# Kernel tuning notes

Measured on AMD Instinct MI355X. Metric: run time of the kernel, lower is better.

The kernel has to match this reference:

```python
import jax, jax.numpy as jnp
import numpy as np

B, T, V, E, H = 256, 512, 50000, 300, 128
NORM_GAIN = 0.8     # norm_gain fed at train time
FORGET_BIAS = 1.0
EPS = 1e-12         # tf.contrib.layers.layer_norm default epsilon


def setup_inputs() -> dict:
    key = jax.random.key(0)
    k1, k2, k3 = jax.random.split(key, 3)
    x = jax.random.randint(k1, (B, T), 0, V, dtype=jnp.int32)
    embed = jax.random.normal(k2, (V, E), dtype=jnp.float32)  # tf.random_normal stddev=1
    W = jax.random.normal(k3, (E + H, 4 * H), dtype=jnp.float32) / np.float32(np.sqrt(E + H))
    gains = jnp.full((5, H), NORM_GAIN, dtype=jnp.float32)   # i, j, f, o, cell-transform
    shifts = jnp.zeros((5, H), dtype=jnp.float32)
    return {"x": x, "embed": embed, "W": W, "gains": gains, "shifts": shifts}


def _ln(v, g, b):
    # layer norm over feature axis with learned gain/shift
    m = jnp.mean(v, axis=-1, keepdims=True)
    var = jnp.mean(jnp.square(v - m), axis=-1, keepdims=True)
    return (v - m) * jax.lax.rsqrt(var + EPS) * g + b


def reference(x, embed, W, gains, shifts):
    # embedding: einsum('abc,cd->abd', one_hot(x), embed) == embed[x]
    xe = jnp.take(embed, x, axis=0)            # [B, T, E]
    xe = jnp.transpose(xe, (1, 0, 2))          # [T, B, E] for scan
    c0 = jnp.zeros((x.shape[0], H), jnp.float32)
    h0 = c0

    def step(carry, x_t):
        c, h = carry
        z = jnp.concatenate([x_t, h], axis=-1) @ W      # [B, 4H], no bias
        i, j, f, o = jnp.split(z, 4, axis=-1)
        i = _ln(i, gains[0], shifts[0])
        j = _ln(j, gains[1], shifts[1])
        f = _ln(f, gains[2], shifts[2])
        o = _ln(o, gains[3], shifts[3])
        g = jax.nn.relu(j)                              # activation=tf.nn.relu
        new_c = c * jax.nn.sigmoid(f + FORGET_BIAS) + jax.nn.sigmoid(i) * g
        new_h = jax.nn.relu(_ln(new_c, gains[4], shifts[4])) * jax.nn.sigmoid(o)
        return (new_c, new_h), new_h

    _, ys = jax.lax.scan(step, (c0, h0), xe)            # ys: [T, B, H]
    return jnp.transpose(ys, (1, 0, 2))                 # [B, T, H]
```

## Files before the change

### kernel.cpp

```cpp
#include <hip/hip_runtime.h>
#include <math.h>

#define Bb   256
#define Tt   512
#define Vv   50000
#define Ee   300
#define Hh   128
#define G4   512
#define EPS  1e-12f
#define FBIAS 1.0f

typedef _Float16 half8 __attribute__((ext_vector_type(8)));
typedef float    f32x4 __attribute__((ext_vector_type(4)));

template <int CTRL>
__device__ inline float dpp_mov(float v) {
    return __int_as_float(
        __builtin_amdgcn_update_dpp(0, __float_as_int(v), CTRL, 0xF, 0xF, true));
}
__device__ inline float red16(float v) {
    v += dpp_mov<0xB1>(v);
    v += dpp_mov<0x4E>(v);
    v += dpp_mov<0x141>(v);
    v += dpp_mov<0x140>(v);
    return v;
}
__device__ inline float red64b(float v) {
    v = red16(v);
    v += dpp_mov<0x142>(v);
    v += dpp_mov<0x143>(v);
    return __int_as_float(__builtin_amdgcn_readlane(__float_as_int(v), 63));
}

__device__ inline void lds_barrier() {
    __builtin_amdgcn_sched_barrier(0);
    asm volatile("s_waitcnt lgkmcnt(0)" ::: "memory");
    __builtin_amdgcn_sched_barrier(0);
    __builtin_amdgcn_s_barrier();
    __builtin_amdgcn_sched_barrier(0);
}

__device__ inline float sigm(float v) {
    return __fdividef(1.0f, 1.0f + __expf(-v));
}

#define PROJ_TILES ((Vv + 31) / 32)

__global__ __launch_bounds__(512, 2) void embed_proj_mfma(
    const float* __restrict__ embed,
    const float* __restrict__ W,
    _Float16* __restrict__ P)
{
    __shared__ __align__(16) _Float16 A[32 * 320];

    const int tid  = threadIdx.x;
    const int wv   = tid >> 6;
    const int lane = tid & 63;
    const int p16  = lane & 15;
    const int gq   = lane >> 4;

    half8 bf[4][10];
    #pragma unroll
    for (int tt = 0; tt < 4; ++tt) {
        #pragma unroll
        for (int ks = 0; ks < 10; ++ks) {
            half8 h;
            #pragma unroll
            for (int j = 0; j < 8; ++j) {
                int k = ks * 32 + gq * 8 + j;
                h[j] = (k < Ee)
                     ? (_Float16)W[(size_t)k * G4 + wv * 64 + tt * 16 + p16]
                     : (_Float16)0.f;
            }
            bf[tt][ks] = h;
        }
    }

    char* const Ab = (char*)A;
    for (int i = tid; i < 32 * 10; i += 512) {
        int row = i / 10, m = i - row * 10;
        *(uint*)(Ab + ((row * 640 + 600 + m * 4) ^ ((row & 7) << 4))) = 0u;
    }
    __syncthreads();

    for (int mtile = blockIdx.x; mtile < PROJ_TILES; mtile += gridDim.x) {
        const int r0 = mtile * 32;

        for (int i = tid; i < 32 * 75; i += 512) {
            int row = i / 75, k4 = i - row * 75;
            int grow = r0 + row;
            float4 v = (grow < Vv) ? *(const float4*)&embed[(size_t)grow * Ee + k4 * 4]
                                   : (float4){0.f, 0.f, 0.f, 0.f};
            union { _Float16 h[4]; uint2 u; } pk;
            pk.h[0] = (_Float16)v.x; pk.h[1] = (_Float16)v.y;
            pk.h[2] = (_Float16)v.z; pk.h[3] = (_Float16)v.w;
            *(uint2*)(Ab + ((row * 640 + k4 * 8) ^ ((row & 7) << 4))) = pk.u;
        }
        __syncthreads();

        f32x4 acc[2][4];
        #pragma unroll
        for (int mt = 0; mt < 2; ++mt)
            #pragma unroll
            for (int tt = 0; tt < 4; ++tt)
                acc[mt][tt] = (f32x4){0.f, 0.f, 0.f, 0.f};

        #pragma unroll
        for (int mt = 0; mt < 2; ++mt) {
            const int arow = mt * 16 + p16;
            #pragma unroll
            for (int ks = 0; ks < 10; ++ks) {
                half8 af = *(const half8*)(Ab + ((arow * 640 + ks * 64 + gq * 16)
                                                 ^ ((arow & 7) << 4)));
                #pragma unroll
                for (int tt = 0; tt < 4; ++tt)
                    acc[mt][tt] = __builtin_amdgcn_mfma_f32_16x16x32_f16(
                        af, bf[tt][ks], acc[mt][tt], 0, 0, 0);
            }
        }

        #pragma unroll
        for (int mt = 0; mt < 2; ++mt)
            #pragma unroll
            for (int tt = 0; tt < 4; ++tt)
                #pragma unroll
                for (int r = 0; r < 4; ++r) {
                    int row = r0 + mt * 16 + gq * 4 + r;
                    if (row < Vv)
                        P[(size_t)row * G4 + wv * 64 + tt * 16 + p16] =
                            (_Float16)acc[mt][tt][r];
                }
        __syncthreads();
    }
}

#define RPBLK 4
#define LBLK  (Bb / RPBLK)

#define LSTM_STEP(TSTEP, PC, PL)                                               \
{                                                                              \
              \
    {                                                                          \
        const _Float16* pr = P + (size_t)tkR * G4;                             \
        _Pragma("unroll")                                                      \
        for (int g = 0; g < 4; ++g)                                            \
            PL[g] = *(const uint*)&pr[g * 128 + 2 * lane];                     \
    }                                                                          \
    {                                                                          \
        half8 af[4];                                                           \
        _Pragma("unroll")                                                      \
        for (int ks = 0; ks < 4; ++ks)                                         \
            af[ks] = *(const half8*)(hb + p16 * 256 +                          \
                         ((ks * 64 + (gq << 4)) ^ ((p16 & 7) << 4)));          \
        f32x4 acc[8];                                                          \
        _Pragma("unroll")                                                      \
        for (int tt = 0; tt < 8; ++tt) acc[tt] = (f32x4){0.f, 0.f, 0.f, 0.f};  \
        _Pragma("unroll")                                                      \
        for (int tt = 0; tt < 8; ++tt) {                                       \
            _Pragma("unroll")                                                  \
            for (int ks = 0; ks < 4; ++ks)                                     \
                acc[tt] = __builtin_amdgcn_mfma_f32_16x16x32_f16(              \
                    af[ks], bfrag[tt][ks], acc[tt], 0, 0, 0);                  \
        }                                                                      \
        if (lane < 16) {                                                       \
            _Pragma("unroll")                                                  \
            for (int g = 0; g < 4; ++g) {                                      \
                _Pragma("unroll")                                              \
                for (int hh = 0; hh < 2; ++hh) {                               \
                    const int tt  = g * 2 + hh;                                \
                    const int col = g * 128 + wv * 32 + hh * 16 + p16;         \
                    _Pragma("unroll")                                          \
                    for (int r = 0; r < 4; ++r) z_lds[r][col] = acc[tt][r];    \
                }                                                              \
            }                                                                  \
        }                                                                      \
    }                                                                          \
    lds_barrier();                                               \
          \
    {                                                                          \
        tkR = xtok[wv][((TSTEP) + 3 < Tt) ? (TSTEP) + 3 : Tt - 1];             \
        float2 zi[4];                                                          \
        _Pragma("unroll")                                                      \
        for (int g = 0; g < 4; ++g) {                                          \
            union { uint u; _Float16 h[2]; } pk; pk.u = PC[g];                 \
            float2 zr = *(const float2*)&z_lds[wv][g * 128 + 2 * lane];        \
            zi[g].x = zr.x + (float)pk.h[0];                                   \
            zi[g].y = zr.y + (float)pk.h[1];                                   \
        }                                                                      \
        float mean[4], rstd[4];                                                \
        _Pragma("unroll")                                                      \
        for (int g = 0; g < 4; ++g) {                                          \
            float s = red64b(zi[g].x + zi[g].y);                               \
            float q = red64b(fmaf(zi[g].x, zi[g].x, zi[g].y * zi[g].y));       \
            mean[g] = s * (1.0f / Hh);                                         \
            float var = q * (1.0f / Hh) - mean[g] * mean[g];                   \
            rstd[g] = rsqrtf(var + EPS);                                       \
        }                                                                      \
        float2 nv[4];                                                          \
        _Pragma("unroll")                                                      \
        for (int g = 0; g < 4; ++g) {                                          \
            nv[g].x = (zi[g].x - mean[g]) * rstd[g] * gg[g].x + sg[g].x;       \
            nv[g].y = (zi[g].y - mean[g]) * rstd[g] * gg[g].y + sg[g].y;       \
        }                                                                      \
        c0 = c0 * sigm(nv[2].x + FBIAS) + sigm(nv[0].x) * fmaxf(nv[1].x, 0.f); \
        c1 = c1 * sigm(nv[2].y + FBIAS) + sigm(nv[0].y) * fmaxf(nv[1].y, 0.f); \
        float s2 = red64b(c0 + c1);                                            \
        float q2 = red64b(fmaf(c0, c0, c1 * c1));                              \
        const float m2 = s2 * (1.0f / Hh);                                     \
        const float v2 = q2 * (1.0f / Hh) - m2 * m2;                           \
        const float r2 = rsqrtf(v2 + EPS);                                     \
        const float lc0 = (c0 - m2) * r2 * gcell.x + scell.x;                  \
        const float lc1 = (c1 - m2) * r2 * gcell.y + scell.y;                  \
        const float h0 = fmaxf(lc0, 0.f) * sigm(nv[3].x);                      \
        const float h1 = fmaxf(lc1, 0.f) * sigm(nv[3].y);                      \
        {                                                                      \
            union { _Float16 hh2[2]; uint u; } pk;                             \
            pk.hh2[0] = (_Float16)h0; pk.hh2[1] = (_Float16)h1;                \
            *(uint*)(hb + wv * 256 + ((4 * lane) ^ ((wv & 7) << 4))) = pk.u;   \
        }                                                                      \
        *(float2*)&out[((size_t)row_g * Tt + (TSTEP)) * Hh + 2 * lane] =       \
            (float2){h0, h1};                                                  \
    }                                                                          \
    lds_barrier();                                                \
}

__global__ __launch_bounds__(256, 1) void lstm_mfma5(
    const _Float16* __restrict__ P,
    const float* __restrict__ W,
    const int*   __restrict__ x,
    const float* __restrict__ gains,
    const float* __restrict__ shifts,
    float* __restrict__ out)
{
    __shared__ __align__(16) float    z_lds[RPBLK][G4];
    __shared__ __align__(16) _Float16 h_lds[16][Hh];
    __shared__ __align__(16) int      xtok[RPBLK][Tt];

    const int tid  = threadIdx.x;
    const int wv   = tid >> 6;
    const int lane = tid & 63;
    const int gq   = lane >> 4;
    const int p16  = lane & 15;
    const int bb   = blockIdx.x;

    {
        const int4* xs = (const int4*)(x + (size_t)bb * RPBLK * Tt);
        int4* xd = (int4*)&xtok[0][0];
        for (int i = tid; i < 512; i += 256) xd[i] = xs[i];
    }

    {
        uint* hz = (uint*)h_lds;
        #pragma unroll
        for (int i = 0; i < 4; ++i) hz[tid + 256 * i] = 0u;
    }

    half8 bfrag[8][4];
    #pragma unroll
    for (int g = 0; g < 4; ++g) {
        #pragma unroll
        for (int hh = 0; hh < 2; ++hh) {
            #pragma unroll
            for (int ks = 0; ks < 4; ++ks) {
                half8 h;
                #pragma unroll
                for (int j = 0; j < 8; ++j) {
                    h[j] = (_Float16)W[(size_t)(Ee + ks * 32 + gq * 8 + j) * G4
                                       + g * 128 + wv * 32 + hh * 16 + p16];
                }
                bfrag[g * 2 + hh][ks] = h;
            }
        }
    }

    float2 gg[4], sg[4];
    #pragma unroll
    for (int g = 0; g < 4; ++g) {
        gg[g] = *(const float2*)&gains[g * Hh + 2 * lane];
        sg[g] = *(const float2*)&shifts[g * Hh + 2 * lane];
    }
    const float2 gcell = *(const float2*)&gains[4 * Hh + 2 * lane];
    const float2 scell = *(const float2*)&shifts[4 * Hh + 2 * lane];

    const int row_g = bb * RPBLK + wv;

    float c0 = 0.f, c1 = 0.f;
    char* const hb = (char*)h_lds;

    __syncthreads();

    uint pA[4], pB[4], pC[4];
    int tkR;
    {
        int tk0 = xtok[wv][0];
        int tk1 = xtok[wv][1];
        tkR = xtok[wv][2];
        const _Float16* p0 = P + (size_t)tk0 * G4;
        const _Float16* p1 = P + (size_t)tk1 * G4;
        #pragma unroll
        for (int g = 0; g < 4; ++g) {
            pA[g] = *(const uint*)&p0[g * 128 + 2 * lane];
            pB[g] = *(const uint*)&p1[g * 128 + 2 * lane];
        }
    }

    for (int t = 0; t < 510; t += 3) {
        LSTM_STEP(t,     pA, pC)
        LSTM_STEP(t + 1, pB, pA)
        LSTM_STEP(t + 2, pC, pB)
    }
    LSTM_STEP(510, pA, pC)
    LSTM_STEP(511, pB, pA)
}

extern "C" void kernel_launch(void* const* d_in, const int* in_sizes, int n_in,
                              void* d_out, int out_size, void* d_ws, size_t ws_size,
                              hipStream_t stream) {
    const int*   x      = (const int*)d_in[0];
    const float* embed  = (const float*)d_in[1];
    const float* W      = (const float*)d_in[2];
    const float* gains  = (const float*)d_in[3];
    const float* shifts = (const float*)d_in[4];
    float* out = (float*)d_out;

    _Float16* P = (_Float16*)d_ws;

    embed_proj_mfma<<<dim3(256), dim3(512), 0, stream>>>(embed, W, P);
    lstm_mfma5<<<dim3(LBLK), dim3(256), 0, stream>>>(P, W, x, gains, shifts, out);
}
```

Measured before the change: 794.2 us.

## Precompute gate row sums to drop per-step mean reductions in LSTM

Two new kernels precompute per-gate column sums of the recurrent weights and per-token gate sums of the projected embeddings. Inside the recurrent step, the gate means come from an extra MFMA of h against the summed weights plus the precomputed token sums, so four of the eight cross-lane DPP reductions are removed. The prefetch depth also grows from three to four steps, and the sched_barriers around the LDS barrier are dropped. The cost is two extra small launches, a pass over P to build Psum, and fp16 rounding of the summed weights, which changes how the mean is computed numerically.

```diff
diff --git a/kernel.cpp b/kernel.cpp
--- a/kernel.cpp
+++ b/kernel.cpp
@@ -33,11 +33,8 @@
 }
 
 __device__ inline void lds_barrier() {
-    __builtin_amdgcn_sched_barrier(0);
     asm volatile("s_waitcnt lgkmcnt(0)" ::: "memory");
-    __builtin_amdgcn_sched_barrier(0);
     __builtin_amdgcn_s_barrier();
-    __builtin_amdgcn_sched_barrier(0);
 }
 
 __device__ inline float sigm(float v) {
@@ -134,10 +131,44 @@
     }
 }
 
+__global__ __launch_bounds__(128) void wsum_kernel(
+    const float* __restrict__ W, float* __restrict__ Wsum)
+{
+    const int k = threadIdx.x;
+    const float* wr = W + (size_t)(Ee + k) * G4;
+    #pragma unroll
+    for (int g = 0; g < 4; ++g) {
+        float s = 0.f;
+        for (int c = 0; c < 128; c += 4) {
+            float4 v = *(const float4*)&wr[g * 128 + c];
+            s += (v.x + v.y) + (v.z + v.w);
+        }
+        Wsum[k * 4 + g] = s;
+    }
+}
+
+__global__ __launch_bounds__(256) void psum_kernel(
+    const _Float16* __restrict__ P, float* __restrict__ Psum)
+{
+    const int lane = threadIdx.x & 63;
+    const int wid  = (blockIdx.x * 256 + threadIdx.x) >> 6;
+    const int nw   = (gridDim.x * 256) >> 6;
+    const int g    = lane >> 4;
+
+    for (int row = wid; row < Vv; row += nw) {
+        half8 v = *(const half8*)&P[(size_t)row * G4 + lane * 8];
+        float s = 0.f;
+        #pragma unroll
+        for (int j = 0; j < 8; ++j) s += (float)v[j];
+        s = red16(s);
+        if ((lane & 15) == 0) Psum[row * 4 + g] = s;
+    }
+}
+
 #define RPBLK 4
 #define LBLK  (Bb / RPBLK)
 
-#define LSTM_STEP(TSTEP, PC, PL)                                               \
+#define LSTM_STEP(TSTEP, PC, QC, PL, QL)                                       \
 {                                                                              \
               \
     {                                                                          \
@@ -145,7 +176,9 @@
         _Pragma("unroll")                                                      \
         for (int g = 0; g < 4; ++g)                                            \
             PL[g] = *(const uint*)&pr[g * 128 + 2 * lane];                     \
+        QL = *(const float4*)&Psum[(size_t)tkR * 4];                           \
     }                                                                          \
+    f32x4 acc_s = (f32x4){0.f, 0.f, 0.f, 0.f};                                 \
     {                                                                          \
         half8 af[4];                                                           \
         _Pragma("unroll")                                                      \
@@ -162,6 +195,10 @@
                 acc[tt] = __builtin_amdgcn_mfma_f32_16x16x32_f16(              \
                     af[ks], bfrag[tt][ks], acc[tt], 0, 0, 0);                  \
         }                                                                      \
+        _Pragma("unroll")                                                      \
+        for (int ks = 0; ks < 4; ++ks)                                         \
+            acc_s = __builtin_amdgcn_mfma_f32_16x16x32_f16(                    \
+                af[ks], bsum[ks], acc_s, 0, 0, 0);                             \
         if (lane < 16) {                                                       \
             _Pragma("unroll")                                                  \
             for (int g = 0; g < 4; ++g) {                                      \
@@ -178,7 +215,7 @@
     lds_barrier();                                               \
           \
     {                                                                          \
-        tkR = xtok[wv][((TSTEP) + 3 < Tt) ? (TSTEP) + 3 : Tt - 1];             \
+        tkR = xtok[wv][((TSTEP) + 4 < Tt) ? (TSTEP) + 4 : Tt - 1];             \
         float2 zi[4];                                                          \
         _Pragma("unroll")                                                      \
         for (int g = 0; g < 4; ++g) {                                          \
@@ -187,12 +224,24 @@
             zi[g].x = zr.x + (float)pk.h[0];                                   \
             zi[g].y = zr.y + (float)pk.h[1];                                   \
         }                                                                      \
+              \
+        float sr = acc_s[0];                                                   \
+        sr = (wv == 1) ? acc_s[1] : sr;                                        \
+        sr = (wv == 2) ? acc_s[2] : sr;                                        \
+        sr = (wv == 3) ? acc_s[3] : sr;                                        \
         float mean[4], rstd[4];                                                \
+        {                                                                      \
+            const float qs[4] = {QC.x, QC.y, QC.z, QC.w};                      \
+            _Pragma("unroll")                                                  \
+            for (int g = 0; g < 4; ++g) {                                      \
+                float sg_ = __int_as_float(                                    \
+                    __builtin_amdgcn_readlane(__float_as_int(sr), g));         \
+                mean[g] = (qs[g] + sg_) * (1.0f / Hh);                         \
+            }                                                                  \
+        }                                                                      \
         _Pragma("unroll")                                                      \
         for (int g = 0; g < 4; ++g) {                                          \
-            float s = red64b(zi[g].x + zi[g].y);                               \
             float q = red64b(fmaf(zi[g].x, zi[g].x, zi[g].y * zi[g].y));       \
-            mean[g] = s * (1.0f / Hh);                                         \
             float var = q * (1.0f / Hh) - mean[g] * mean[g];                   \
             rstd[g] = rsqrtf(var + EPS);                                       \
         }                                                                      \
@@ -202,6 +251,8 @@
             nv[g].x = (zi[g].x - mean[g]) * rstd[g] * gg[g].x + sg[g].x;       \
             nv[g].y = (zi[g].y - mean[g]) * rstd[g] * gg[g].y + sg[g].y;       \
         }                                                                      \
+        const float sox = sigm(nv[3].x);                \
+        const float soy = sigm(nv[3].y);                                       \
         c0 = c0 * sigm(nv[2].x + FBIAS) + sigm(nv[0].x) * fmaxf(nv[1].x, 0.f); \
         c1 = c1 * sigm(nv[2].y + FBIAS) + sigm(nv[0].y) * fmaxf(nv[1].y, 0.f); \
         float s2 = red64b(c0 + c1);                                            \
@@ -211,8 +262,8 @@
         const float r2 = rsqrtf(v2 + EPS);                                     \
         const float lc0 = (c0 - m2) * r2 * gcell.x + scell.x;                  \
         const float lc1 = (c1 - m2) * r2 * gcell.y + scell.y;                  \
-        const float h0 = fmaxf(lc0, 0.f) * sigm(nv[3].x);                      \
-        const float h1 = fmaxf(lc1, 0.f) * sigm(nv[3].y);                      \
+        const float h0 = fmaxf(lc0, 0.f) * sox;                                \
+        const float h1 = fmaxf(lc1, 0.f) * soy;                                \
         {                                                                      \
             union { _Float16 hh2[2]; uint u; } pk;                             \
             pk.hh2[0] = (_Float16)h0; pk.hh2[1] = (_Float16)h1;                \
@@ -224,8 +275,10 @@
     lds_barrier();                                                \
 }
 
-__global__ __launch_bounds__(256, 1) void lstm_mfma5(
+__global__ __launch_bounds__(256, 1) void lstm_mfma6(
     const _Float16* __restrict__ P,
+    const float* __restrict__ Psum,
+    const float* __restrict__ Wsum,
     const float* __restrict__ W,
     const int*   __restrict__ x,
     const float* __restrict__ gains,
@@ -273,6 +326,16 @@
         }
     }
 
+    half8 bsum[4];
+    #pragma unroll
+    for (int ks = 0; ks < 4; ++ks) {
+        half8 h;
+        #pragma unroll
+        for (int j = 0; j < 8; ++j)
+            h[j] = (_Float16)Wsum[(ks * 32 + gq * 8 + j) * 4 + (p16 & 3)];
+        bsum[ks] = h;
+    }
+
     float2 gg[4], sg[4];
     #pragma unroll
     for (int g = 0; g < 4; ++g) {
@@ -289,28 +352,34 @@
 
     __syncthreads();
 
-    uint pA[4], pB[4], pC[4];
+    uint pA[4], pB[4], pC[4], pD[4];
+    float4 qA, qB, qC, qD;
     int tkR;
     {
         int tk0 = xtok[wv][0];
         int tk1 = xtok[wv][1];
-        tkR = xtok[wv][2];
+        int tk2 = xtok[wv][2];
+        tkR = xtok[wv][3];
         const _Float16* p0 = P + (size_t)tk0 * G4;
         const _Float16* p1 = P + (size_t)tk1 * G4;
+        const _Float16* p2 = P + (size_t)tk2 * G4;
         #pragma unroll
         for (int g = 0; g < 4; ++g) {
             pA[g] = *(const uint*)&p0[g * 128 + 2 * lane];
             pB[g] = *(const uint*)&p1[g * 128 + 2 * lane];
-        }
-    }
-
-    for (int t = 0; t < 510; t += 3) {
-        LSTM_STEP(t,     pA, pC)
-        LSTM_STEP(t + 1, pB, pA)
-        LSTM_STEP(t + 2, pC, pB)
-    }
-    LSTM_STEP(510, pA, pC)
-    LSTM_STEP(511, pB, pA)
+            pC[g] = *(const uint*)&p2[g * 128 + 2 * lane];
+        }
+        qA = *(const float4*)&Psum[(size_t)tk0 * 4];
+        qB = *(const float4*)&Psum[(size_t)tk1 * 4];
+        qC = *(const float4*)&Psum[(size_t)tk2 * 4];
+    }
+
+    for (int t = 0; t < Tt; t += 4) {
+        LSTM_STEP(t,     pA, qA, pD, qD)
+        LSTM_STEP(t + 1, pB, qB, pA, qA)
+        LSTM_STEP(t + 2, pC, qC, pB, qB)
+        LSTM_STEP(t + 3, pD, qD, pC, qC)
+    }
 }
 
 extern "C" void kernel_launch(void* const* d_in, const int* in_sizes, int n_in,
@@ -323,8 +392,13 @@
     const float* shifts = (const float*)d_in[4];
     float* out = (float*)d_out;
 
-    _Float16* P = (_Float16*)d_ws;
+    _Float16* P    = (_Float16*)d_ws;
+    float*    Psum = (float*)((char*)d_ws + (size_t)Vv * G4 * 2);
+    float*    Wsum = (float*)((char*)Psum + (size_t)Vv * 4 * 4);
 
     embed_proj_mfma<<<dim3(256), dim3(512), 0, stream>>>(embed, W, P);
-    lstm_mfma5<<<dim3(LBLK), dim3(256), 0, stream>>>(P, W, x, gains, shifts, out);
-}
+    wsum_kernel<<<dim3(1), dim3(128), 0, stream>>>(W, Wsum);
+    psum_kernel<<<dim3(412), dim3(256), 0, stream>>>(P, Psum);
+    lstm_mfma6<<<dim3(LBLK), dim3(256), 0, stream>>>(P, Psum, Wsum, W, x,
+                                                     gains, shifts, out);
+}
```

Result: no change. 788.6 us (-0.7%).
